# Kernel optimization log

Measured on AMD Instinct MI355X. Metric: run time of the kernel, lower is better.

## Reference

```python
import jax, jax.numpy as jnp
import numpy as np

VOCAB, EMB, MAXPOS, HID, IMG, ATT = 30522, 768, 512, 512, 2048, 256
LN_EPS = 1e-12


def bert_embed(ids, word_emb, pos_emb, type_emb, ln_g, ln_b):
    # ids: [..., L]; BERT embeddings = word + position + token_type(0), then LayerNorm
    L = ids.shape[-1]
    x = word_emb[ids] + pos_emb[:L] + type_emb[0]
    mu = jnp.mean(x, axis=-1, keepdims=True)
    var = jnp.mean((x - mu) ** 2, axis=-1, keepdims=True)
    return ln_g * (x - mu) * jax.lax.rsqrt(var + LN_EPS) + ln_b


def setup_inputs() -> dict:
    key = jax.random.key(0)
    ks = jax.random.split(key, 24)
    B, L, S, H = 32, 512, 6, 128
    u = lambda k, shape: jax.random.uniform(k, shape, jnp.float32, -0.1, 0.1)
    inp = {
        "separate_images": jax.random.normal(ks[0], (B, S, IMG), jnp.float32),
        "img_pred": jax.random.normal(ks[1], (B, IMG), jnp.float32),
        "input_text": jax.random.randint(ks[2], (B, L), 0, VOCAB),
        "prev_hist": jax.random.randint(ks[3], (B, S, H), 0, VOCAB),
        "prev_hist_len": jax.random.randint(ks[4], (B, S), 0, H),
        "masks": jnp.zeros((B, L), dtype=bool),
        # BERT embedding params
        "word_emb": jax.random.normal(ks[5], (VOCAB, EMB), jnp.float32) * 0.02,
        "pos_emb": jax.random.normal(ks[6], (MAXPOS, EMB), jnp.float32) * 0.02,
        "type_emb": jax.random.normal(ks[7], (2, EMB), jnp.float32) * 0.02,
        "ln_g": jnp.ones((EMB,), jnp.float32),
        "ln_b": jnp.zeros((EMB,), jnp.float32),
        # model linears (weights stored input-major: [in, out])
        "W_sep": u(ks[8], (IMG, HID)), "b_sep": jnp.zeros((HID,), jnp.float32),
        "W_e2h": u(ks[9], (EMB, HID)), "b_e2h": jnp.zeros((HID,), jnp.float32),
        "W_hist": u(ks[10], (EMB, HID)), "b_hist": jnp.zeros((HID,), jnp.float32),
        "W_img": u(ks[11], (IMG, HID)), "b_img": jnp.zeros((HID,), jnp.float32),
        "W_mm": u(ks[12], (2 * HID, HID)), "b_mm": jnp.zeros((HID,), jnp.float32),
        "W_a1": u(ks[13], (HID, ATT)), "b_a1": jnp.zeros((ATT,), jnp.float32),
        "W_a2": u(ks[14], (ATT, 1)), "b_a2": jnp.zeros((1,), jnp.float32),
        "W_f1": u(ks[15], (2 * HID, HID)), "b_f1": jnp.zeros((HID,), jnp.float32),
        "W_f2": u(ks[16], (HID, 2)), "b_f2": jnp.zeros((2,), jnp.float32),
    }
    return inp


def reference(separate_images, img_pred, input_text, prev_hist, prev_hist_len, masks,
              word_emb, pos_emb, type_emb, ln_g, ln_b,
              W_sep, b_sep, W_e2h, b_e2h, W_hist, b_hist, W_img, b_img,
              W_mm, b_mm, W_a1, b_a1, W_a2, b_a2, W_f1, b_f1, W_f2, b_f2):
    relu = jax.nn.relu
    # utterance path
    reps = bert_embed(input_text, word_emb, pos_emb, type_emb, ln_g, ln_b)  # [B,L,E]
    input_reps = relu(reps @ W_e2h + b_e2h)                                 # [B,L,H]
    proj_img = relu(img_pred @ W_img + b_img)                               # [B,H]
    rep_img = jnp.broadcast_to(proj_img[:, None, :], input_reps.shape)
    mm_reps = relu(jnp.concatenate([input_reps, rep_img], axis=2) @ W_mm + b_mm)
    att = jnp.tanh(mm_reps @ W_a1 + b_a1) @ W_a2 + b_a2                     # [B,L,1]
    att = jnp.where(masks[:, :, None], -jnp.inf, att)
    w = jax.nn.softmax(att, axis=1)
    attended = jnp.sum(mm_reps * w, axis=1)                                 # [B,H]
    # image / history path
    sep = separate_images @ W_sep + b_sep                                   # [B,6,H]
    H = prev_hist.shape[-1]
    hist_emb = bert_embed(prev_hist, word_emb, pos_emb, type_emb, ln_g, ln_b)  # [B,6,Hl,E]
    valid = (jnp.arange(H) < prev_hist_len[..., None]).astype(hist_emb.dtype)  # [B,6,Hl]
    denom = jnp.maximum(prev_hist_len, 1).astype(hist_emb.dtype)[..., None]
    hist_avg = jnp.einsum('bshe,bsh->bse', hist_emb, valid) / denom
    contrib = relu(hist_avg @ W_hist + b_hist) * (prev_hist_len[..., None] > 0)
    sep = relu(sep + contrib)
    sep = sep / jnp.maximum(jnp.linalg.norm(sep, axis=2, keepdims=True), 1e-12)
    sep = sep.mean(axis=1)                                                  # [B,H]
    h = jnp.concatenate([sep, attended], axis=1) @ W_f1 + b_f1
    h = jax.nn.gelu(h, approximate=False)
    return h @ W_f2 + b_f2
```

## Files before the change

### kernel.cpp

```cpp
#include <hip/hip_runtime.h>
#include <hip/hip_bf16.h>
#include <math.h>

#define VOCAB 30522
#define EMB 768
#define MAXPOS 512
#define HID 512
#define IMG 2048
#define ATT 256
#define BB 32
#define LL 512
#define SS 6
#define HL 128
#define LN_EPS 1e-12f
#define KCH 128
#define NROWS (BB * LL)
#define MPS (BB + BB * SS)

typedef __bf16 bf16_t;
typedef __attribute__((ext_vector_type(4))) __bf16 bf16x4;
typedef __attribute__((ext_vector_type(8))) __bf16 bf16x8;
typedef __attribute__((ext_vector_type(4))) float f32x4;

#define AS1 __attribute__((address_space(1)))
#define AS3 __attribute__((address_space(3)))
__device__ __forceinline__ void gload_lds16(const bf16_t* g, bf16_t* l) {
    __builtin_amdgcn_global_load_lds((const AS1 void*)g, (AS3 void*)l, 16, 0, 0);
}

__device__ __forceinline__ float wave_sum(float v) {
    v += __shfl_xor(v, 1);  v += __shfl_xor(v, 2);  v += __shfl_xor(v, 4);
    v += __shfl_xor(v, 8);  v += __shfl_xor(v, 16); v += __shfl_xor(v, 32);
    return v;
}
__device__ __forceinline__ float wave_max(float v) {
    v = fmaxf(v, __shfl_xor(v, 1));  v = fmaxf(v, __shfl_xor(v, 2));
    v = fmaxf(v, __shfl_xor(v, 4));  v = fmaxf(v, __shfl_xor(v, 8));
    v = fmaxf(v, __shfl_xor(v, 16)); v = fmaxf(v, __shfl_xor(v, 32));
    return v;
}


__device__ void dev_embed(int r, const int* __restrict__ ids,
                          const float* __restrict__ we, const float* __restrict__ pe,
                          const float* __restrict__ te, const float* __restrict__ g,
                          const float* __restrict__ bta, bf16_t* __restrict__ out) {
    int lane = threadIdx.x & 63;
    int l = r & (LL - 1);
    int id = ids[r];
    const float* wrow = we + (size_t)id * EMB + lane * 12;
    const float* prow = pe + (size_t)l * EMB + lane * 12;
    const float* tp = te + lane * 12;
    float x[12]; float s = 0.f, ss = 0.f;
#pragma unroll
    for (int q = 0; q < 3; q++) {
        float4 a = *(const float4*)(wrow + q * 4);
        float4 b = *(const float4*)(prow + q * 4);
        float4 c = *(const float4*)(tp + q * 4);
        float v0 = a.x + b.x + c.x, v1 = a.y + b.y + c.y;
        float v2 = a.z + b.z + c.z, v3 = a.w + b.w + c.w;
        x[q * 4 + 0] = v0; x[q * 4 + 1] = v1; x[q * 4 + 2] = v2; x[q * 4 + 3] = v3;
        s += v0 + v1 + v2 + v3;
        ss += v0 * v0 + v1 * v1 + v2 * v2 + v3 * v3;
    }
    s = wave_sum(s); ss = wave_sum(ss);
    float mu = s * (1.0f / EMB);
    float var = ss * (1.0f / EMB) - mu * mu;
    float rs = rsqrtf(var + LN_EPS);
    bf16_t* orow = out + (size_t)r * EMB + lane * 12;
    const float* gp = g + lane * 12;
    const float* bp = bta + lane * 12;
#pragma unroll
    for (int q = 0; q < 3; q++) {
        float4 gv = *(const float4*)(gp + q * 4);
        float4 bv = *(const float4*)(bp + q * 4);
        bf16x4 y;
        y[0] = (bf16_t)(gv.x * (x[q * 4 + 0] - mu) * rs + bv.x);
        y[1] = (bf16_t)(gv.y * (x[q * 4 + 1] - mu) * rs + bv.y);
        y[2] = (bf16_t)(gv.z * (x[q * 4 + 2] - mu) * rs + bv.z);
        y[3] = (bf16_t)(gv.w * (x[q * 4 + 3] - mu) * rs + bv.w);
        *(bf16x4*)(orow + q * 4) = y;
    }
}

__device__ void dev_conv(const float* __restrict__ in, bf16_t* __restrict__ out,
                         int K, int N, int x, int y, char* smem) {
    float (*t)[33] = (float(*)[33])smem;
    int n0 = x * 32, k0 = y * 32;
    int tx = threadIdx.x & 31, ty = threadIdx.x >> 5;
#pragma unroll
    for (int i = 0; i < 4; i++)
        t[ty + i * 8][tx] = in[(size_t)(k0 + ty + i * 8) * N + n0 + tx];
    __syncthreads();
#pragma unroll
    for (int i = 0; i < 4; i++)
        out[(size_t)(n0 + ty + i * 8) * K + k0 + tx] = (bf16_t)t[tx][ty + i * 8];
}

__device__ void dev_hist(int bs, int grp, const int* __restrict__ ids,
                         const int* __restrict__ lens,
                         const float* __restrict__ we, const float* __restrict__ pe,
                         const float* __restrict__ te, const float* __restrict__ g,
                         const float* __restrict__ bta,
                         float* __restrict__ parts, char* smem) {
    float (*acc)[EMB] = (float(*)[EMB])smem;
    int len = lens[bs];
    int tid = threadIdx.x, wid = tid >> 6, lane = tid & 63;
#pragma unroll
    for (int k = 0; k < 12; k++) acc[wid][lane + k * 64] = 0.f;
#pragma unroll
    for (int i = 0; i < 4; i++) {
        int h = grp + 8 * wid + 32 * i;
        if (h >= len) continue;
        int id = ids[bs * HL + h];
        const float* wrow = we + (size_t)id * EMB;
        const float* prow = pe + (size_t)h * EMB;
        float x[12]; float s = 0.f, ss = 0.f;
#pragma unroll
        for (int k = 0; k < 12; k++) {
            int j = lane + k * 64;
            float v = wrow[j] + prow[j] + te[j];
            x[k] = v; s += v; ss += v * v;
        }
        s = wave_sum(s); ss = wave_sum(ss);
        float mu = s * (1.0f / EMB);
        float var = ss * (1.0f / EMB) - mu * mu;
        float rs = rsqrtf(var + LN_EPS);
#pragma unroll
        for (int k = 0; k < 12; k++) {
            int j = lane + k * 64;
            acc[wid][j] += g[j] * (x[k] - mu) * rs + bta[j];
        }
    }
    __syncthreads();
    float* dst = parts + ((size_t)grp * (BB * SS) + bs) * EMB;
    for (int j = tid; j < EMB; j += 256)
        dst[j] = acc[0][j] + acc[1][j] + acc[2][j] + acc[3][j];
}

template <int AMODE>
__device__ void dev_thin(int bx, int by, int bz,
                         const float* __restrict__ A, int lda,
                         const float* __restrict__ parts, size_t MNp,
                         const float* __restrict__ abias,
                         const int* __restrict__ lens,
                         const float* __restrict__ B, int ldb,
                         float* __restrict__ part, int M, int N, char* smem) {
    float (*As)[KCH] = (float(*)[KCH])smem;
    int tid = threadIdx.x;
    int n0 = bx * 256, m0 = by * 16, k0 = bz * KCH;

    if (AMODE == 0) {
#pragma unroll
        for (int i = 0; i < 2; i++) {
            int lin = (i * 256 + tid) * 4;
            int m = lin >> 7, k = lin & (KCH - 1);
            *(float4*)&As[m][k] = *(const float4*)(A + (size_t)(m0 + m) * lda + k0 + k);
        }
    } else if (AMODE == 1) {
#pragma unroll
        for (int i = 0; i < 2; i++) {
            int f = i * 256 + tid;
            int m = f >> 5, kq = (f & 31) * 4;
            int row = m0 + m;
            float4 v = *(const float4*)(abias + k0 + kq);
#pragma unroll
            for (int ks = 0; ks < 16; ks++) {
                float4 p = *(const float4*)(parts + (size_t)ks * MNp +
                                            (size_t)row * 512 + k0 + kq);
                v.x += p.x; v.y += p.y; v.z += p.z; v.w += p.w;
            }
            v.x = fmaxf(v.x, 0.f); v.y = fmaxf(v.y, 0.f);
            v.z = fmaxf(v.z, 0.f); v.w = fmaxf(v.w, 0.f);
            *(float4*)&As[m][kq] = v;
        }
    } else {
#pragma unroll
        for (int i = 0; i < 2; i++) {
            int f = i * 256 + tid;
            int m = f >> 5, kq = (f & 31) * 4;
            int row = m0 + m;
            float invd = 1.0f / fmaxf((float)lens[row], 1.0f);
            float4 v = {};
#pragma unroll
            for (int g = 0; g < 8; g++) {
                float4 p = *(const float4*)(parts + (size_t)g * MNp +
                                            (size_t)row * EMB + k0 + kq);
                v.x += p.x; v.y += p.y; v.z += p.z; v.w += p.w;
            }
            As[m][kq + 0] = v.x * invd; As[m][kq + 1] = v.y * invd;
            As[m][kq + 2] = v.z * invd; As[m][kq + 3] = v.w * invd;
        }
    }
    __syncthreads();
    int nq = tid & 63, mg = tid >> 6;
    const float* Bp = B + (size_t)k0 * ldb + n0 + nq * 4;
    float4 acc[4] = {};
    for (int kk = 0; kk < KCH; kk += 8) {
        float4 b0 = *(const float4*)(Bp + (size_t)(kk + 0) * ldb);
        float4 b1 = *(const float4*)(Bp + (size_t)(kk + 1) * ldb);
        float4 b2 = *(const float4*)(Bp + (size_t)(kk + 2) * ldb);
        float4 b3 = *(const float4*)(Bp + (size_t)(kk + 3) * ldb);
        float4 b4 = *(const float4*)(Bp + (size_t)(kk + 4) * ldb);
        float4 b5 = *(const float4*)(Bp + (size_t)(kk + 5) * ldb);
        float4 b6 = *(const float4*)(Bp + (size_t)(kk + 6) * ldb);
        float4 b7 = *(const float4*)(Bp + (size_t)(kk + 7) * ldb);
        float4 bv[8] = {b0, b1, b2, b3, b4, b5, b6, b7};
#pragma unroll
        for (int j = 0; j < 8; j++) {
#pragma unroll
            for (int mi = 0; mi < 4; mi++) {
                float a = As[mg * 4 + mi][kk + j];
                acc[mi].x += a * bv[j].x; acc[mi].y += a * bv[j].y;
                acc[mi].z += a * bv[j].z; acc[mi].w += a * bv[j].w;
            }
        }
    }
    size_t MN = (size_t)M * N;
#pragma unroll
    for (int mi = 0; mi < 4; mi++)
        *(float4*)(part + (size_t)bz * MN +
                   (size_t)(m0 + mg * 4 + mi) * N + n0 + nq * 4) = acc[mi];
}

template <int ACT, bool OBF16, bool ROWADD4, bool FUSE_ATT>
__device__ void dev_mfma(int bx, int by,
                         const bf16_t* __restrict__ A, const bf16_t* __restrict__ Bt,
                         const float* __restrict__ bias,
                         const float* __restrict__ rowadd,
                         void* __restrict__ Cv,
                         const float* __restrict__ w2, float* __restrict__ att_part,
                         int M, int N, int K, char* smem) {
    bf16_t* As = (bf16_t*)smem;
    bf16_t* Bs = (bf16_t*)(smem + 16384);
    float (*attp)[2] = (float(*)[2])(smem + 32768);
    int tid = threadIdx.x;
    int lane = tid & 63, wid = tid >> 6;
    int wr = wid >> 1, wc = wid & 1;
    int row0 = by * 128, col0 = bx * 128;

    int srow = tid >> 2;
    int sslot = tid & 3;

    const bf16_t* Ag = A + (size_t)row0 * K;
    const bf16_t* Bg = Bt + (size_t)col0 * K;

    f32x4 acc[4][4] = {};
    int lrow = lane & 15;
    int g8 = lane >> 4;

    auto stage_pair = [&](int buf, int kb) {
#pragma unroll
        for (int rr = 0; rr < 2; rr++) {
            int r = srow + rr * 64;
            int sl = sslot ^ ((r >> 1) & 3);
            gload_lds16(Ag + (size_t)r * K + kb + sl * 8,
                        As + buf * 4096 + wid * 512 + rr * 2048);
            gload_lds16(Bg + (size_t)r * K + kb + sl * 8,
                        Bs + buf * 4096 + wid * 512 + rr * 2048);
        }
    };

    stage_pair(0, 0);
    __syncthreads();
    int cur = 0;
    for (int kb = 0; kb < K; kb += 32) {
        if (kb + 32 < K) stage_pair(cur ^ 1, kb + 32);
        bf16x8 af[4], bfr[4];
#pragma unroll
        for (int mi = 0; mi < 4; mi++) {
            int r = wr * 64 + mi * 16 + lrow;
            int sl = g8 ^ ((r >> 1) & 3);
            af[mi] = *(const bf16x8*)(As + cur * 4096 + r * 32 + sl * 8);
        }
#pragma unroll
        for (int ni = 0; ni < 4; ni++) {
            int r = wc * 64 + ni * 16 + lrow;
            int sl = g8 ^ ((r >> 1) & 3);
            bfr[ni] = *(const bf16x8*)(Bs + cur * 4096 + r * 32 + sl * 8);
        }
#pragma unroll
        for (int mi = 0; mi < 4; mi++)
#pragma unroll
            for (int ni = 0; ni < 4; ni++)
                acc[mi][ni] = __builtin_amdgcn_mfma_f32_16x16x32_bf16(
                    af[mi], bfr[ni], acc[mi][ni], 0, 0, 0);
        __syncthreads();
        cur ^= 1;
    }

    if (FUSE_ATT) {
        float w2v[4];
#pragma unroll
        for (int ni = 0; ni < 4; ni++)
            w2v[ni] = w2[col0 + wc * 64 + ni * 16 + lrow];
#pragma unroll
        for (int mi = 0; mi < 4; mi++) {
#pragma unroll
            for (int r = 0; r < 4; r++) {
                float s = 0.f;
#pragma unroll
                for (int ni = 0; ni < 4; ni++) {
                    int col = col0 + wc * 64 + ni * 16 + lrow;
                    float v = tanhf(acc[mi][ni][r] + bias[col]);
                    s += v * w2v[ni];
                }
                s += __shfl_xor(s, 1); s += __shfl_xor(s, 2);
                s += __shfl_xor(s, 4); s += __shfl_xor(s, 8);
                if ((lane & 15) == 0)
                    attp[wr * 64 + mi * 16 + (lane >> 4) * 4 + r][wc] = s;
            }
        }
        __syncthreads();
        if (tid < 128)
            att_part[(size_t)bx * M + row0 + tid] = attp[tid][0] + attp[tid][1];
        return;
    }

    float* Cf = (float*)Cv;
    bf16_t* Cb = (bf16_t*)Cv;
    int rg = (lane >> 4) * 4;
#pragma unroll
    for (int mi = 0; mi < 4; mi++) {
#pragma unroll
        for (int ni = 0; ni < 4; ni++) {
            int col = col0 + wc * 64 + ni * 16 + lrow;
#pragma unroll
            for (int r = 0; r < 4; r++) {
                int row = row0 + wr * 64 + mi * 16 + rg + r;
                float v = acc[mi][ni][r] + bias[col];
                if (ROWADD4) {
                    int bslot = row >> 9;
#pragma unroll
                    for (int ks = 0; ks < 4; ks++)
                        v += rowadd[(size_t)ks * BB * HID + (size_t)bslot * HID + col];
                }
                if (ACT == 1) v = fmaxf(v, 0.f);
                if (ACT == 2) v = tanhf(v);
                if (OBF16) Cb[(size_t)row * N + col] = (bf16_t)v;
                else       Cf[(size_t)row * N + col] = v;
            }
        }
    }
}


#define D1_EMB   4096
#define D1_HIST  (D1_EMB + 1536)
#define D1_CONV  (D1_HIST + 768)
#define D1_T4A   (D1_CONV + 64)
#define D1_T4B   (D1_T4A + 384)
__global__ __launch_bounds__(256)
void uber_pre(const int* input_text, const int* prev_hist, const int* prev_hist_ln,
              const float* word_emb, const float* pos_emb, const float* type_emb,
              const float* ln_g, const float* ln_b,
              const float* W_e2h, bf16_t* Wt_e2h,
              const float* W_mm, bf16_t* Wt_mm,
              const float* W_a1, bf16_t* Wt_a1,
              const float* img_pred, const float* sep_images,
              const float* W_img, const float* W_sep,
              bf16_t* reps_bf, float* hist_parts, float* partA) {
    __shared__ __align__(16) char smem[12288];
    int bid = blockIdx.x;
    if (bid < D1_EMB) {
        int r = bid * 4 + (threadIdx.x >> 6);
        dev_embed(r, input_text, word_emb, pos_emb, type_emb, ln_g, ln_b, reps_bf);
    } else if (bid < D1_HIST) {
        int b = bid - D1_EMB;
        dev_hist(b >> 3, b & 7, prev_hist, prev_hist_ln, word_emb, pos_emb,
                 type_emb, ln_g, ln_b, hist_parts, smem);
    } else if (bid < D1_CONV) {
        int b = bid - D1_HIST;
        if (b < 384)      dev_conv(W_e2h, Wt_e2h, EMB, HID, b & 15, b >> 4, smem);
        else if (b < 640) { int c = b - 384; dev_conv(W_mm, Wt_mm, HID, HID, c & 15, c >> 4, smem); }
        else              { int c = b - 640; dev_conv(W_a1, Wt_a1, HID, ATT, c & 7, c >> 3, smem); }
    } else if (bid < D1_T4A) {
        int l = bid - D1_CONV;
        dev_thin<0>(l & 1, (l >> 1) & 1, l >> 2, img_pred, IMG,
                    nullptr, 0, nullptr, nullptr, W_img, HID, partA, MPS, HID, smem);
    } else {
        int l = bid - D1_T4A;
        int l2 = l >> 1;
        dev_thin<0>(l & 1, l2 % 12, l2 / 12, sep_images, IMG,
                    nullptr, 0, nullptr, nullptr, W_sep, HID,
                    partA + (size_t)BB * HID, MPS, HID, smem);
    }
}

#define D2_MF   512
#define D2_IMG2 (D2_MF + 16)
#define D2_HG   (D2_IMG2 + 144)
__global__ __launch_bounds__(256)
void uber_gemm1(const bf16_t* reps_bf, const bf16_t* Wt_e2h, const float* b_e2h,
                bf16_t* input_reps,
                const float* partA, const float* b_img, const float* W_mm,
                float* partC,
                const float* hist_parts, const int* prev_hist_ln,
                const float* W_hist, float* partB) {
    __shared__ __align__(16) char smem[33792];
    int bid = blockIdx.x;
    if (bid < D2_MF) {
        dev_mfma<1, true, false, false>(bid & 3, bid >> 2, reps_bf, Wt_e2h, b_e2h,
                                        nullptr, input_reps, nullptr, nullptr,
                                        NROWS, HID, EMB, smem);
    } else if (bid < D2_IMG2) {
        int l = bid - D2_MF;
        dev_thin<1>(l & 1, (l >> 1) & 1, l >> 2, nullptr, 0,
                    partA, (size_t)MPS * HID, b_img, nullptr,
                    W_mm + (size_t)HID * HID, HID, partC, BB, HID, smem);
    } else {
        int l = bid - D2_IMG2;
        int l2 = l >> 1;
        dev_thin<2>(l & 1, l2 % 12, l2 / 12, nullptr, 0,
                    hist_parts, (size_t)BB * SS * EMB, nullptr, prev_hist_ln,
                    W_hist, HID, partB, BB * SS, HID, smem);
    }
}

__global__ __launch_bounds__(256)
void mfma_mm_k(const bf16_t* input_reps, const bf16_t* Wt_mm, const float* b_mm,
               const float* partC, bf16_t* mm_reps) {
    __shared__ __align__(16) char smem[33792];
    dev_mfma<1, true, true, false>(blockIdx.x & 3, blockIdx.x >> 2, input_reps,
                                   Wt_mm, b_mm, partC, mm_reps, nullptr, nullptr,
                                   NROWS, HID, HID, smem);
}

__global__ __launch_bounds__(256)
void mfma_a1_k(const bf16_t* mm_reps, const bf16_t* Wt_a1, const float* b_a1,
               const float* W_a2, float* att_part) {
    __shared__ __align__(16) char smem[33792];
    dev_mfma<2, false, false, true>(blockIdx.x & 1, blockIdx.x >> 1, mm_reps,
                                    Wt_a1, b_a1, nullptr, nullptr, W_a2, att_part,
                                    NROWS, ATT, HID, smem);
}

__global__ void attend_sep(const float* __restrict__ att_part,
                           const unsigned char* __restrict__ masks,
                           const float* __restrict__ b2,
                           const bf16_t* __restrict__ mm,
                           const float* __restrict__ pA,
                           const float* __restrict__ pB,
                           const float* __restrict__ b_sep,
                           const float* __restrict__ b_hist,
                           const int* __restrict__ lens,
                           float* __restrict__ xcat) {
    int bid = blockIdx.x;
    int tid = threadIdx.x, wid = tid >> 6, lane = tid & 63;
    __shared__ float wsm[LL];
    __shared__ float arr[4];
    __shared__ float red[4][64];
    if (bid < 256) {
        int b = bid >> 3, hc = bid & 7;
        int l0 = tid, l1 = tid + 256;
        float v0 = att_part[b * LL + l0] + att_part[(size_t)NROWS + b * LL + l0] + b2[0];
        float v1 = att_part[b * LL + l1] + att_part[(size_t)NROWS + b * LL + l1] + b2[0];
        if (masks[b * LL + l0]) v0 = -INFINITY;
        if (masks[b * LL + l1]) v1 = -INFINITY;
        float m = wave_max(fmaxf(v0, v1));
        if (lane == 0) arr[wid] = m;
        __syncthreads();
        float M = fmaxf(fmaxf(arr[0], arr[1]), fmaxf(arr[2], arr[3]));
        float e0 = expf(v0 - M), e1 = expf(v1 - M);
        wsm[l0] = e0; wsm[l1] = e1;
        float s = wave_sum(e0 + e1);
        __syncthreads();
        if (lane == 0) arr[wid] = s;
        __syncthreads();
        float inv = 1.0f / (arr[0] + arr[1] + arr[2] + arr[3]);
        int h = hc * 64 + lane;
        const bf16_t* base = mm + (size_t)b * LL * HID + h;
        float acc = 0.f;
        int ls = wid * 128;
#pragma unroll 4
        for (int l = ls; l < ls + 128; l++)
            acc += (float)base[(size_t)l * HID] * wsm[l];
        red[wid][lane] = acc;
        __syncthreads();
        if (wid == 0)
            xcat[b * 1024 + 512 + h] =
                (red[0][lane] + red[1][lane] + red[2][lane] + red[3][lane]) * inv;
    } else {
        int b = bid - 256;
        const size_t MNa = (size_t)MPS * HID;
        const size_t MNb = (size_t)BB * SS * HID;
        float acc0 = 0.f, acc1 = 0.f;
        for (int s = 0; s < SS; s++) {
            int idx = b * SS + s;
            int len = lens[idx];
            size_t baseA = (size_t)(BB + idx) * HID;
            size_t baseB = (size_t)idx * HID;
            float v0 = b_sep[tid], v1 = b_sep[tid + 256];
#pragma unroll
            for (int ks = 0; ks < 16; ks++) {
                v0 += pA[ks * MNa + baseA + tid];
                v1 += pA[ks * MNa + baseA + tid + 256];
            }
            float c0 = b_hist[tid], c1 = b_hist[tid + 256];
#pragma unroll
            for (int ks = 0; ks < 6; ks++) {
                c0 += pB[ks * MNb + baseB + tid];
                c1 += pB[ks * MNb + baseB + tid + 256];
            }
            c0 = fmaxf(c0, 0.f); c1 = fmaxf(c1, 0.f);
            if (len <= 0) { c0 = 0.f; c1 = 0.f; }
            float y0 = fmaxf(v0 + c0, 0.f), y1 = fmaxf(v1 + c1, 0.f);
            float ssq = wave_sum(y0 * y0 + y1 * y1);
            if (lane == 0) arr[wid] = ssq;
            __syncthreads();
            float tot = arr[0] + arr[1] + arr[2] + arr[3];
            float inv = 1.0f / fmaxf(sqrtf(tot), 1e-12f);
            acc0 += y0 * inv; acc1 += y1 * inv;
            __syncthreads();
        }
        xcat[b * 1024 + tid] = acc0 * (1.0f / SS);
        xcat[b * 1024 + 256 + tid] = acc1 * (1.0f / SS);
    }
}

__global__ __launch_bounds__(256)
void thin_f1_k(const float* xcat, const float* W_f1, float* partD) {
    __shared__ __align__(16) char smem[8192];
    int l = blockIdx.x;
    dev_thin<0>(l & 1, (l >> 1) & 1, l >> 2, xcat, 1024,
                nullptr, 0, nullptr, nullptr, W_f1, HID, partD, BB, HID, smem);
}

__global__ void final_out2(const float* __restrict__ part,
                           const float* __restrict__ b1,
                           const float* __restrict__ W2,
                           const float* __restrict__ b2,
                           float* __restrict__ out) {
    int b = blockIdx.x;
    int tid = threadIdx.x;
    __shared__ float h[HID];
    const size_t MN = (size_t)BB * HID;
#pragma unroll
    for (int jj = 0; jj < 2; jj++) {
        int d = tid + jj * 256;
        float a = b1[d];
#pragma unroll
        for (int ks = 0; ks < 8; ks++) a += part[ks * MN + (size_t)b * HID + d];
        h[d] = 0.5f * a * (1.0f + erff(a * 0.70710678118654752f));
    }
    __syncthreads();
    float p0 = 0.f, p1 = 0.f;
    for (int j = tid; j < HID; j += 256) {
        float hv = h[j];
        p0 += hv * W2[j * 2 + 0];
        p1 += hv * W2[j * 2 + 1];
    }
    p0 = wave_sum(p0); p1 = wave_sum(p1);
    __shared__ float r0[4], r1[4];
    int wid = tid >> 6;
    if ((tid & 63) == 0) { r0[wid] = p0; r1[wid] = p1; }
    __syncthreads();
    if (tid == 0) {
        out[b * 2 + 0] = r0[0] + r0[1] + r0[2] + r0[3] + b2[0];
        out[b * 2 + 1] = r1[0] + r1[1] + r1[2] + r1[3] + b2[1];
    }
}

extern "C" void kernel_launch(void* const* d_in, const int* in_sizes, int n_in,
                              void* d_out, int out_size, void* d_ws, size_t ws_size,
                              hipStream_t stream) {
    const float* sep_images   = (const float*)d_in[0];
    const float* img_pred     = (const float*)d_in[1];
    const int*   input_text   = (const int*)d_in[2];
    const int*   prev_hist    = (const int*)d_in[3];
    const int*   prev_hist_ln = (const int*)d_in[4];
    const unsigned char* masks = (const unsigned char*)d_in[5];
    const float* word_emb = (const float*)d_in[6];
    const float* pos_emb  = (const float*)d_in[7];
    const float* type_emb = (const float*)d_in[8];
    const float* ln_g = (const float*)d_in[9];
    const float* ln_b = (const float*)d_in[10];
    const float* W_sep = (const float*)d_in[11]; const float* b_sep = (const float*)d_in[12];
    const float* W_e2h = (const float*)d_in[13]; const float* b_e2h = (const float*)d_in[14];
    const float* W_hist = (const float*)d_in[15]; const float* b_hist = (const float*)d_in[16];
    const float* W_img = (const float*)d_in[17]; const float* b_img = (const float*)d_in[18];
    const float* W_mm = (const float*)d_in[19]; const float* b_mm = (const float*)d_in[20];
    const float* W_a1 = (const float*)d_in[21]; const float* b_a1 = (const float*)d_in[22];
    const float* W_a2 = (const float*)d_in[23]; const float* b_a2 = (const float*)d_in[24];
    const float* W_f1 = (const float*)d_in[25]; const float* b_f1 = (const float*)d_in[26];
    const float* W_f2 = (const float*)d_in[27]; const float* b_f2 = (const float*)d_in[28];

    char* ws = (char*)d_ws;
    size_t o = 0;
    auto alloc = [&](size_t bytes) { void* p = ws + o; o += (bytes + 255) & ~(size_t)255; return p; };

    bf16_t* reps_bf     = (bf16_t*)alloc((size_t)NROWS * EMB * 2);
    bf16_t* input_reps  = (bf16_t*)alloc((size_t)NROWS * HID * 2);
    bf16_t* mm_reps     = (bf16_t*)alloc((size_t)NROWS * HID * 2);
    float*  att_part    = (float*)alloc((size_t)2 * NROWS * 4);
    float*  xcat        = (float*)alloc((size_t)BB * 1024 * 4);
    float*  hist_parts  = (float*)alloc((size_t)8 * BB * SS * EMB * 4);
    bf16_t* Wt_e2h      = (bf16_t*)alloc((size_t)EMB * HID * 2);
    bf16_t* Wt_mm       = (bf16_t*)alloc((size_t)HID * HID * 2);
    bf16_t* Wt_a1       = (bf16_t*)alloc((size_t)HID * ATT * 2);
    float*  partA       = (float*)alloc((size_t)16 * MPS * HID * 4);
    float*  partB       = (float*)alloc((size_t)6 * BB * SS * HID * 4);
    float*  partC       = (float*)alloc((size_t)4 * BB * HID * 4);
    float*  partD       = (float*)alloc((size_t)8 * BB * HID * 4);

    uber_pre<<<D1_T4B, 256, 0, stream>>>(
        input_text, prev_hist, prev_hist_ln, word_emb, pos_emb, type_emb,
        ln_g, ln_b, W_e2h, Wt_e2h, W_mm, Wt_mm, W_a1, Wt_a1,
        img_pred, sep_images, W_img, W_sep, reps_bf, hist_parts, partA);

    uber_gemm1<<<D2_HG, 256, 0, stream>>>(
        reps_bf, Wt_e2h, b_e2h, input_reps,
        partA, b_img, W_mm, partC,
        hist_parts, prev_hist_ln, W_hist, partB);

    mfma_mm_k<<<512, 256, 0, stream>>>(input_reps, Wt_mm, b_mm, partC, mm_reps);

    mfma_a1_k<<<256, 256, 0, stream>>>(mm_reps, Wt_a1, b_a1, W_a2, att_part);

    attend_sep<<<288, 256, 0, stream>>>(att_part, masks, b_a2, mm_reps,
                                        partA, partB, b_sep, b_hist,
                                        prev_hist_ln, xcat);

    thin_f1_k<<<32, 256, 0, stream>>>(xcat, W_f1, partD);

    final_out2<<<BB, 256, 0, stream>>>(partD, b_f1, W_f2, b_f2, (float*)d_out);
}
```

Baseline: 147.0 us.

## Coalesce embedding loads, enlarge thin-GEMM row tiles, move sep GEMM into gemm1

The embedding and history LayerNorm paths now load float4 values strided by lane, so consecutive lanes read consecutive 16-byte chunks instead of each lane reading a 48-byte contiguous span. The thin GEMM is templated on the row-tile size. The image, sep, hist and f1 GEMMs now use 32- or 64-row tiles, which means each loaded weight chunk is reused across more rows and fewer blocks are launched. The separate-images GEMM moves out of the preprocessing kernel into uber_gemm1, which it does not depend on, to balance work across launches. The trade-off is larger shared-memory tiles: the 64-row tile needs 32KB, and more accumulators per thread mean less parallelism.

```diff
diff --git a/kernel.cpp b/kernel.cpp
--- a/kernel.cpp
+++ b/kernel.cpp
@@ -48,38 +48,38 @@
     int lane = threadIdx.x & 63;
     int l = r & (LL - 1);
     int id = ids[r];
-    const float* wrow = we + (size_t)id * EMB + lane * 12;
-    const float* prow = pe + (size_t)l * EMB + lane * 12;
-    const float* tp = te + lane * 12;
-    float x[12]; float s = 0.f, ss = 0.f;
+    const float4* w4 = (const float4*)(we + (size_t)id * EMB);
+    const float4* p4 = (const float4*)(pe + (size_t)l * EMB);
+    const float4* t4 = (const float4*)te;
+    float4 xv[3]; float s = 0.f, ss = 0.f;
 #pragma unroll
     for (int q = 0; q < 3; q++) {
-        float4 a = *(const float4*)(wrow + q * 4);
-        float4 b = *(const float4*)(prow + q * 4);
-        float4 c = *(const float4*)(tp + q * 4);
-        float v0 = a.x + b.x + c.x, v1 = a.y + b.y + c.y;
-        float v2 = a.z + b.z + c.z, v3 = a.w + b.w + c.w;
-        x[q * 4 + 0] = v0; x[q * 4 + 1] = v1; x[q * 4 + 2] = v2; x[q * 4 + 3] = v3;
-        s += v0 + v1 + v2 + v3;
-        ss += v0 * v0 + v1 * v1 + v2 * v2 + v3 * v3;
+        int j = lane + 64 * q;
+        float4 a = w4[j], b = p4[j], c = t4[j];
+        float4 v;
+        v.x = a.x + b.x + c.x; v.y = a.y + b.y + c.y;
+        v.z = a.z + b.z + c.z; v.w = a.w + b.w + c.w;
+        xv[q] = v;
+        s += v.x + v.y + v.z + v.w;
+        ss += v.x * v.x + v.y * v.y + v.z * v.z + v.w * v.w;
     }
     s = wave_sum(s); ss = wave_sum(ss);
     float mu = s * (1.0f / EMB);
     float var = ss * (1.0f / EMB) - mu * mu;
     float rs = rsqrtf(var + LN_EPS);
-    bf16_t* orow = out + (size_t)r * EMB + lane * 12;
-    const float* gp = g + lane * 12;
-    const float* bp = bta + lane * 12;
+    bf16x4* o4 = (bf16x4*)(out + (size_t)r * EMB);
+    const float4* g4 = (const float4*)g;
+    const float4* b4 = (const float4*)bta;
 #pragma unroll
     for (int q = 0; q < 3; q++) {
-        float4 gv = *(const float4*)(gp + q * 4);
-        float4 bv = *(const float4*)(bp + q * 4);
+        int j = lane + 64 * q;
+        float4 gv = g4[j], bv = b4[j];
         bf16x4 y;
-        y[0] = (bf16_t)(gv.x * (x[q * 4 + 0] - mu) * rs + bv.x);
-        y[1] = (bf16_t)(gv.y * (x[q * 4 + 1] - mu) * rs + bv.y);
-        y[2] = (bf16_t)(gv.z * (x[q * 4 + 2] - mu) * rs + bv.z);
-        y[3] = (bf16_t)(gv.w * (x[q * 4 + 3] - mu) * rs + bv.w);
-        *(bf16x4*)(orow + q * 4) = y;
+        y[0] = (bf16_t)(gv.x * (xv[q].x - mu) * rs + bv.x);
+        y[1] = (bf16_t)(gv.y * (xv[q].y - mu) * rs + bv.y);
+        y[2] = (bf16_t)(gv.z * (xv[q].z - mu) * rs + bv.z);
+        y[3] = (bf16_t)(gv.w * (xv[q].w - mu) * rs + bv.w);
+        o4[j] = y;
     }
 }
 
@@ -106,30 +106,46 @@
     float (*acc)[EMB] = (float(*)[EMB])smem;
     int len = lens[bs];
     int tid = threadIdx.x, wid = tid >> 6, lane = tid & 63;
-#pragma unroll
-    for (int k = 0; k < 12; k++) acc[wid][lane + k * 64] = 0.f;
+    float4* a4 = (float4*)acc[wid];
+    float4 z = {};
+#pragma unroll
+    for (int q = 0; q < 3; q++) a4[lane + 64 * q] = z;
+    const float4* t4 = (const float4*)te;
+    const float4* g4 = (const float4*)g;
+    const float4* b4 = (const float4*)bta;
 #pragma unroll
     for (int i = 0; i < 4; i++) {
         int h = grp + 8 * wid + 32 * i;
         if (h >= len) continue;
         int id = ids[bs * HL + h];
-        const float* wrow = we + (size_t)id * EMB;
-        const float* prow = pe + (size_t)h * EMB;
-        float x[12]; float s = 0.f, ss = 0.f;
-#pragma unroll
-        for (int k = 0; k < 12; k++) {
-            int j = lane + k * 64;
-            float v = wrow[j] + prow[j] + te[j];
-            x[k] = v; s += v; ss += v * v;
+        const float4* w4 = (const float4*)(we + (size_t)id * EMB);
+        const float4* p4 = (const float4*)(pe + (size_t)h * EMB);
+        float4 xv[3]; float s = 0.f, ss = 0.f;
+#pragma unroll
+        for (int q = 0; q < 3; q++) {
+            int j = lane + 64 * q;
+            float4 a = w4[j], b = p4[j], c = t4[j];
+            float4 v;
+            v.x = a.x + b.x + c.x; v.y = a.y + b.y + c.y;
+            v.z = a.z + b.z + c.z; v.w = a.w + b.w + c.w;
+            xv[q] = v;
+            s += v.x + v.y + v.z + v.w;
+            ss += v.x * v.x + v.y * v.y + v.z * v.z + v.w * v.w;
         }
         s = wave_sum(s); ss = wave_sum(ss);
         float mu = s * (1.0f / EMB);
         float var = ss * (1.0f / EMB) - mu * mu;
         float rs = rsqrtf(var + LN_EPS);
 #pragma unroll
-        for (int k = 0; k < 12; k++) {
-            int j = lane + k * 64;
-            acc[wid][j] += g[j] * (x[k] - mu) * rs + bta[j];
+        for (int q = 0; q < 3; q++) {
+            int j = lane + 64 * q;
+            float4 gv = g4[j], bv = b4[j];
+            float4 cu = a4[j];
+            cu.x += gv.x * (xv[q].x - mu) * rs + bv.x;
+            cu.y += gv.y * (xv[q].y - mu) * rs + bv.y;
+            cu.z += gv.z * (xv[q].z - mu) * rs + bv.z;
+            cu.w += gv.w * (xv[q].w - mu) * rs + bv.w;
+            a4[j] = cu;
         }
     }
     __syncthreads();
@@ -138,79 +154,63 @@
         dst[j] = acc[0][j] + acc[1][j] + acc[2][j] + acc[3][j];
 }
 
-template <int AMODE>
-__device__ void dev_thin(int bx, int by, int bz,
-                         const float* __restrict__ A, int lda,
-                         const float* __restrict__ parts, size_t MNp,
-                         const float* __restrict__ abias,
-                         const int* __restrict__ lens,
-                         const float* __restrict__ B, int ldb,
-                         float* __restrict__ part, int M, int N, char* smem) {
+template <int RT, int AMODE>
+__device__ void dev_thin_rt(int bx, int by, int bz,
+                            const float* __restrict__ A, int lda,
+                            const float* __restrict__ parts, size_t MNp,
+                            const float* __restrict__ abias,
+                            const int* __restrict__ lens,
+                            const float* __restrict__ B, int ldb,
+                            float* __restrict__ part, int M, int N, char* smem) {
     float (*As)[KCH] = (float(*)[KCH])smem;
     int tid = threadIdx.x;
-    int n0 = bx * 256, m0 = by * 16, k0 = bz * KCH;
-
-    if (AMODE == 0) {
-#pragma unroll
-        for (int i = 0; i < 2; i++) {
-            int lin = (i * 256 + tid) * 4;
-            int m = lin >> 7, k = lin & (KCH - 1);
-            *(float4*)&As[m][k] = *(const float4*)(A + (size_t)(m0 + m) * lda + k0 + k);
-        }
-    } else if (AMODE == 1) {
-#pragma unroll
-        for (int i = 0; i < 2; i++) {
-            int f = i * 256 + tid;
-            int m = f >> 5, kq = (f & 31) * 4;
-            int row = m0 + m;
-            float4 v = *(const float4*)(abias + k0 + kq);
+    int n0 = bx * 256, m0 = by * RT, k0 = bz * KCH;
+    constexpr int NV = RT * KCH / 1024;
+#pragma unroll
+    for (int i = 0; i < NV; i++) {
+        int lin = (i * 256 + tid) * 4;
+        int m = lin >> 7, k = lin & (KCH - 1);
+        int row = m0 + m;
+        if (AMODE == 0) {
+            *(float4*)&As[m][k] = *(const float4*)(A + (size_t)row * lda + k0 + k);
+        } else if (AMODE == 1) {
+            float4 v = *(const float4*)(abias + k0 + k);
 #pragma unroll
             for (int ks = 0; ks < 16; ks++) {
                 float4 p = *(const float4*)(parts + (size_t)ks * MNp +
-                                            (size_t)row * 512 + k0 + kq);
+                                            (size_t)row * 512 + k0 + k);
                 v.x += p.x; v.y += p.y; v.z += p.z; v.w += p.w;
             }
             v.x = fmaxf(v.x, 0.f); v.y = fmaxf(v.y, 0.f);
             v.z = fmaxf(v.z, 0.f); v.w = fmaxf(v.w, 0.f);
-            *(float4*)&As[m][kq] = v;
-        }
-    } else {
-#pragma unroll
-        for (int i = 0; i < 2; i++) {
-            int f = i * 256 + tid;
-            int m = f >> 5, kq = (f & 31) * 4;
-            int row = m0 + m;
+            *(float4*)&As[m][k] = v;
+        } else {
             float invd = 1.0f / fmaxf((float)lens[row], 1.0f);
             float4 v = {};
 #pragma unroll
-            for (int g = 0; g < 8; g++) {
-                float4 p = *(const float4*)(parts + (size_t)g * MNp +
-                                            (size_t)row * EMB + k0 + kq);
+            for (int gg = 0; gg < 8; gg++) {
+                float4 p = *(const float4*)(parts + (size_t)gg * MNp +
+                                            (size_t)row * EMB + k0 + k);
                 v.x += p.x; v.y += p.y; v.z += p.z; v.w += p.w;
             }
-            As[m][kq + 0] = v.x * invd; As[m][kq + 1] = v.y * invd;
-            As[m][kq + 2] = v.z * invd; As[m][kq + 3] = v.w * invd;
+            As[m][k + 0] = v.x * invd; As[m][k + 1] = v.y * invd;
+            As[m][k + 2] = v.z * invd; As[m][k + 3] = v.w * invd;
         }
     }
     __syncthreads();
     int nq = tid & 63, mg = tid >> 6;
     const float* Bp = B + (size_t)k0 * ldb + n0 + nq * 4;
-    float4 acc[4] = {};
+    float4 acc[RT / 4] = {};
     for (int kk = 0; kk < KCH; kk += 8) {
-        float4 b0 = *(const float4*)(Bp + (size_t)(kk + 0) * ldb);
-        float4 b1 = *(const float4*)(Bp + (size_t)(kk + 1) * ldb);
-        float4 b2 = *(const float4*)(Bp + (size_t)(kk + 2) * ldb);
-        float4 b3 = *(const float4*)(Bp + (size_t)(kk + 3) * ldb);
-        float4 b4 = *(const float4*)(Bp + (size_t)(kk + 4) * ldb);
-        float4 b5 = *(const float4*)(Bp + (size_t)(kk + 5) * ldb);
-        float4 b6 = *(const float4*)(Bp + (size_t)(kk + 6) * ldb);
-        float4 b7 = *(const float4*)(Bp + (size_t)(kk + 7) * ldb);
-        float4 bv[8] = {b0, b1, b2, b3, b4, b5, b6, b7};
+        float4 bv[8];
+#pragma unroll
+        for (int j = 0; j < 8; j++)
+            bv[j] = *(const float4*)(Bp + (size_t)(kk + j) * ldb);
 #pragma unroll
         for (int j = 0; j < 8; j++) {
 #pragma unroll
-            for (int mi = 0; mi < 4; mi++) {
-                float a = As[mg * 4 + mi][kk + j];
+            for (int mi = 0; mi < RT / 4; mi++) {
+                float a = As[mg * (RT / 4) + mi][kk + j];
                 acc[mi].x += a * bv[j].x; acc[mi].y += a * bv[j].y;
                 acc[mi].z += a * bv[j].z; acc[mi].w += a * bv[j].w;
             }
@@ -218,9 +218,9 @@
     }
     size_t MN = (size_t)M * N;
 #pragma unroll
-    for (int mi = 0; mi < 4; mi++)
+    for (int mi = 0; mi < RT / 4; mi++)
         *(float4*)(part + (size_t)bz * MN +
-                   (size_t)(m0 + mg * 4 + mi) * N + n0 + nq * 4) = acc[mi];
+                   (size_t)(m0 + mg * (RT / 4) + mi) * N + n0 + nq * 4) = acc[mi];
 }
 
 template <int ACT, bool OBF16, bool ROWADD4, bool FUSE_ATT>
@@ -348,8 +348,7 @@
 #define D1_EMB   4096
 #define D1_HIST  (D1_EMB + 1536)
 #define D1_CONV  (D1_HIST + 768)
-#define D1_T4A   (D1_CONV + 64)
-#define D1_T4B   (D1_T4A + 384)
+#define D1_TIMG  (D1_CONV + 32)
 __global__ __launch_bounds__(256)
 void uber_pre(const int* input_text, const int* prev_hist, const int* prev_hist_ln,
               const float* word_emb, const float* pos_emb, const float* type_emb,
@@ -357,10 +356,9 @@
               const float* W_e2h, bf16_t* Wt_e2h,
               const float* W_mm, bf16_t* Wt_mm,
               const float* W_a1, bf16_t* Wt_a1,
-              const float* img_pred, const float* sep_images,
-              const float* W_img, const float* W_sep,
+              const float* img_pred, const float* W_img,
               bf16_t* reps_bf, float* hist_parts, float* partA) {
-    __shared__ __align__(16) char smem[12288];
+    __shared__ __align__(16) char smem[16384];
     int bid = blockIdx.x;
     if (bid < D1_EMB) {
         int r = bid * 4 + (threadIdx.x >> 6);
@@ -374,26 +372,23 @@
         if (b < 384)      dev_conv(W_e2h, Wt_e2h, EMB, HID, b & 15, b >> 4, smem);
         else if (b < 640) { int c = b - 384; dev_conv(W_mm, Wt_mm, HID, HID, c & 15, c >> 4, smem); }
         else              { int c = b - 640; dev_conv(W_a1, Wt_a1, HID, ATT, c & 7, c >> 3, smem); }
-    } else if (bid < D1_T4A) {
+    } else {
         int l = bid - D1_CONV;
-        dev_thin<0>(l & 1, (l >> 1) & 1, l >> 2, img_pred, IMG,
-                    nullptr, 0, nullptr, nullptr, W_img, HID, partA, MPS, HID, smem);
-    } else {
-        int l = bid - D1_T4A;
-        int l2 = l >> 1;
-        dev_thin<0>(l & 1, l2 % 12, l2 / 12, sep_images, IMG,
-                    nullptr, 0, nullptr, nullptr, W_sep, HID,
-                    partA + (size_t)BB * HID, MPS, HID, smem);
+        dev_thin_rt<32, 0>(l & 1, 0, l >> 1, img_pred, IMG,
+                           nullptr, 0, nullptr, nullptr, W_img, HID,
+                           partA, MPS, HID, smem);
     }
 }
 
 #define D2_MF   512
-#define D2_IMG2 (D2_MF + 16)
-#define D2_HG   (D2_IMG2 + 144)
+#define D2_SEP  (D2_MF + 96)
+#define D2_IMG2 (D2_SEP + 16)
+#define D2_HG   (D2_IMG2 + 36)
 __global__ __launch_bounds__(256)
 void uber_gemm1(const bf16_t* reps_bf, const bf16_t* Wt_e2h, const float* b_e2h,
                 bf16_t* input_reps,
-                const float* partA, const float* b_img, const float* W_mm,
+                const float* sep_images, const float* W_sep,
+                float* partA, const float* b_img, const float* W_mm,
                 float* partC,
                 const float* hist_parts, const int* prev_hist_ln,
                 const float* W_hist, float* partB) {
@@ -403,17 +398,23 @@
         dev_mfma<1, true, false, false>(bid & 3, bid >> 2, reps_bf, Wt_e2h, b_e2h,
                                         nullptr, input_reps, nullptr, nullptr,
                                         NROWS, HID, EMB, smem);
+    } else if (bid < D2_SEP) {
+        int l = bid - D2_MF;
+        int l2 = l >> 1;
+        dev_thin_rt<64, 0>(l & 1, l2 % 3, l2 / 3, sep_images, IMG,
+                           nullptr, 0, nullptr, nullptr, W_sep, HID,
+                           partA + (size_t)BB * HID, MPS, HID, smem);
     } else if (bid < D2_IMG2) {
-        int l = bid - D2_MF;
-        dev_thin<1>(l & 1, (l >> 1) & 1, l >> 2, nullptr, 0,
-                    partA, (size_t)MPS * HID, b_img, nullptr,
-                    W_mm + (size_t)HID * HID, HID, partC, BB, HID, smem);
+        int l = bid - D2_SEP;
+        dev_thin_rt<16, 1>(l & 1, (l >> 1) & 1, l >> 2, nullptr, 0,
+                           partA, (size_t)MPS * HID, b_img, nullptr,
+                           W_mm + (size_t)HID * HID, HID, partC, BB, HID, smem);
     } else {
         int l = bid - D2_IMG2;
         int l2 = l >> 1;
-        dev_thin<2>(l & 1, l2 % 12, l2 / 12, nullptr, 0,
-                    hist_parts, (size_t)BB * SS * EMB, nullptr, prev_hist_ln,
-                    W_hist, HID, partB, BB * SS, HID, smem);
+        dev_thin_rt<64, 2>(l & 1, l2 % 3, l2 / 3, nullptr, 0,
+                           hist_parts, (size_t)BB * SS * EMB, nullptr, prev_hist_ln,
+                           W_hist, HID, partB, BB * SS, HID, smem);
     }
 }
 
@@ -520,10 +521,10 @@
 
 __global__ __launch_bounds__(256)
 void thin_f1_k(const float* xcat, const float* W_f1, float* partD) {
-    __shared__ __align__(16) char smem[8192];
+    __shared__ __align__(16) char smem[16384];
     int l = blockIdx.x;
-    dev_thin<0>(l & 1, (l >> 1) & 1, l >> 2, xcat, 1024,
-                nullptr, 0, nullptr, nullptr, W_f1, HID, partD, BB, HID, smem);
+    dev_thin_rt<32, 0>(l & 1, 0, l >> 1, xcat, 1024,
+                       nullptr, 0, nullptr, nullptr, W_f1, HID, partD, BB, HID, smem);
 }
 
 __global__ void final_out2(const float* __restrict__ part,
@@ -603,14 +604,14 @@
     float*  partC       = (float*)alloc((size_t)4 * BB * HID * 4);
     float*  partD       = (float*)alloc((size_t)8 * BB * HID * 4);
 
-    uber_pre<<<D1_T4B, 256, 0, stream>>>(
+    uber_pre<<<D1_TIMG, 256, 0, stream>>>(
         input_text, prev_hist, prev_hist_ln, word_emb, pos_emb, type_emb,
         ln_g, ln_b, W_e2h, Wt_e2h, W_mm, Wt_mm, W_a1, Wt_a1,
-        img_pred, sep_images, W_img, W_sep, reps_bf, hist_parts, partA);
+        img_pred, W_img, reps_bf, hist_parts, partA);
 
     uber_gemm1<<<D2_HG, 256, 0, stream>>>(
         reps_bf, Wt_e2h, b_e2h, input_reps,
-        partA, b_img, W_mm, partC,
+        sep_images, W_sep, partA, b_img, W_mm, partC,
         hist_parts, prev_hist_ln, W_hist, partB);
 
     mfma_mm_k<<<512, 256, 0, stream>>>(input_reps, Wt_mm, b_mm, partC, mm_reps);
@@ -621,7 +622,7 @@
                                         partA, partB, b_sep, b_hist,
                                         prev_hist_ln, xcat);
 
-    thin_f1_k<<<32, 256, 0, stream>>>(xcat, W_f1, partD);
+    thin_f1_k<<<16, 256, 0, stream>>>(xcat, W_f1, partD);
 
     final_out2<<<BB, 256, 0, stream>>>(partD, b_f1, W_f2, b_f2, (float*)d_out);
 }
```

Measured after the change: 186.8 us. 27.0% more time.
